# Kernel tuning notes

Hardware: AMD Instinct MI355X
Metric: run time of the kernel (lower is better)

Reference implementation:

```python
import jax, jax.numpy as jnp
import numpy as np

N_NODES = 20000
N_EDGES = 160000
N_GRAPHS = 64
IN_DIM = 128
HID = 512
N_ACT = 32


def gcn_conv(x, W, b, src, dst, n_nodes):
    # PyG GCNConv: add self-loops, symmetric normalization, x @ W then scatter-add.
    loop = jnp.arange(n_nodes, dtype=src.dtype)
    s = jnp.concatenate([src, loop])
    d = jnp.concatenate([dst, loop])
    deg = jax.ops.segment_sum(jnp.ones_like(d, dtype=x.dtype), d, num_segments=n_nodes)
    dinv = jnp.where(deg > 0, jax.lax.rsqrt(deg), 0.0)
    norm = dinv[s] * dinv[d]                      # [E+N]
    h = x @ W                                     # [N, out]
    msg = h[s] * norm[:, None]                    # gather + scale
    out = jax.ops.segment_sum(msg, d, num_segments=n_nodes)
    return out + b


def setup_inputs() -> dict:
    key = jax.random.key(0)
    ks = jax.random.split(key, 16)
    tree_x = jax.random.normal(ks[0], (N_NODES, IN_DIM), dtype=jnp.float32)
    edge_index = jax.random.randint(ks[1], (2, N_EDGES), 0, N_NODES, dtype=jnp.int32)
    # batch assignment: guarantee every graph id appears, then sort
    raw = jnp.concatenate([jnp.arange(N_GRAPHS, dtype=jnp.int32),
                           jax.random.randint(ks[2], (N_NODES - N_GRAPHS,), 0, N_GRAPHS, dtype=jnp.int32)])
    batch = jnp.sort(raw)

    def glorot(k, shape):
        lim = np.sqrt(6.0 / (shape[0] + shape[1]))
        return jax.random.uniform(k, shape, jnp.float32, -lim, lim)

    params = {
        'W1': glorot(ks[3], (IN_DIM, HID)), 'b1': jnp.zeros((HID,), jnp.float32),
        'W2': glorot(ks[4], (HID, HID)),    'b2': jnp.zeros((HID,), jnp.float32),
        'W3': glorot(ks[5], (HID, HID)),    'b3': jnp.zeros((HID,), jnp.float32),
        'Wf1': glorot(ks[6], (HID, HID)),   'bf1': jnp.zeros((HID,), jnp.float32),
        'Wf2': glorot(ks[7], (HID, HID)),   'bf2': jnp.zeros((HID,), jnp.float32),
        'Wf3': glorot(ks[8], (HID, HID)),   'bf3': jnp.zeros((HID,), jnp.float32),
        'Wo': glorot(ks[9], (HID, N_ACT)),  'bo': jnp.zeros((N_ACT,), jnp.float32),
    }
    return {'tree_x': tree_x, 'edge_index': edge_index, 'batch': batch, **params}


def reference(tree_x, edge_index, batch, W1, b1, W2, b2, W3, b3,
              Wf1, bf1, Wf2, bf2, Wf3, bf3, Wo, bo):
    src, dst = edge_index[0], edge_index[1]
    h = jax.nn.relu(gcn_conv(tree_x, W1, b1, src, dst, N_NODES))
    h = jax.nn.relu(gcn_conv(h, W2, b2, src, dst, N_NODES))
    h = jax.nn.relu(gcn_conv(h, W3, b3, src, dst, N_NODES))
    x = jax.ops.segment_max(h, batch, num_segments=N_GRAPHS)  # global_max_pool
    x = jax.nn.relu(x @ Wf1 + bf1)
    x = jax.nn.relu(x @ Wf2 + bf2)
    x = jax.nn.relu(x @ Wf3 + bf3)
    return x @ Wo + bo
```

## Files before the change

kernel.cpp:

```cpp
#include <hip/hip_runtime.h>
#include <stdint.h>

#define N_NODES 20000
#define N_EDGES 160000
#define N_GRAPHS 64
#define IN_DIM 128
#define HID 512
#define N_ACT 32

#define SCAN_NB ((N_NODES + 255) / 256)

typedef __attribute__((ext_vector_type(8))) short short8;
typedef __attribute__((ext_vector_type(4))) float f32x4;

__device__ __forceinline__ float bf2f(uint h16) {
    union { uint u; float f; } v; v.u = h16 << 16; return v.f;
}
__device__ __forceinline__ float bflo(uint u) {
    union { uint x; float f; } v; v.x = u << 16; return v.f;
}
__device__ __forceinline__ float bfhi(uint u) {
    union { uint x; float f; } v; v.x = u & 0xffff0000u; return v.f;
}
__device__ __forceinline__ ushort f2bf(float f) {
    union { float f; uint u; } v; v.f = f;
    uint u = v.u;
    uint r = (u + 0x7fffu + ((u >> 16) & 1u)) >> 16;
    return (ushort)r;
}


#define PB_HIST   625
#define PB_F2BF   (PB_HIST + 10000)
#define PB_WT1    (PB_F2BF + 256)
#define PB_WT2    (PB_WT1 + 1024)
#define PB_WT3    (PB_WT2 + 1024)
#define PB_BOUNDS (PB_WT3 + SCAN_NB)

__global__ __launch_bounds__(256) void k_prep(
    const int* __restrict__ edst, int* __restrict__ cnt,
    const float* __restrict__ tree_x, ushort* __restrict__ xbf,
    const float* __restrict__ W1, ushort* __restrict__ w1t,
    const float* __restrict__ W2, ushort* __restrict__ w2t,
    const float* __restrict__ W3, ushort* __restrict__ w3t,
    const int* __restrict__ batch, int* __restrict__ gstart)
{
    int b = blockIdx.x;
    int t = threadIdx.x;
    if (b < PB_HIST) {
        int e = b * 256 + t;
        if (e < N_EDGES) atomicAdd(&cnt[edst[e]], 1);
    } else if (b < PB_F2BF) {
        int i = (b - PB_HIST) * 256 + t;
        if (i < N_NODES * IN_DIM) xbf[i] = f2bf(tree_x[i]);
    } else if (b < PB_WT1) {
        int i = (b - PB_F2BF) * 256 + t;
        int n = i / IN_DIM, k = i % IN_DIM;
        w1t[i] = f2bf(W1[k * HID + n]);
    } else if (b < PB_WT2) {
        int i = (b - PB_WT1) * 256 + t;
        int n = i / HID, k = i % HID;
        w2t[i] = f2bf(W2[k * HID + n]);
    } else if (b < PB_WT3) {
        int i = (b - PB_WT2) * 256 + t;
        int n = i / HID, k = i % HID;
        w3t[i] = f2bf(W3[k * HID + n]);
    } else {
        int i = (b - PB_WT3) * 256 + t;
        if (i < N_NODES) {
            if (i == 0) {
                gstart[batch[0]] = 0;
                gstart[N_GRAPHS] = N_NODES;
            } else if (batch[i] != batch[i - 1]) {
                gstart[batch[i]] = i;
            }
        }
    }
}


__global__ __launch_bounds__(256) void k_part(const int* __restrict__ cnt, int* __restrict__ bsum) {
    __shared__ int s[256];
    int idx = blockIdx.x * 256 + threadIdx.x;
    s[threadIdx.x] = (idx < N_NODES) ? cnt[idx] : 0;
    __syncthreads();
    for (int off = 128; off > 0; off >>= 1) {
        if (threadIdx.x < off) s[threadIdx.x] += s[threadIdx.x + off];
        __syncthreads();
    }
    if (threadIdx.x == 0) bsum[blockIdx.x] = s[0];
}

__global__ __launch_bounds__(128) void k_scanb(const int* __restrict__ bsum,
                                               int* __restrict__ boff, int* __restrict__ rowstart) {
    __shared__ int s[128];
    int t = threadIdx.x;
    int own = (t < SCAN_NB) ? bsum[t] : 0;
    s[t] = own;
    __syncthreads();
    for (int off = 1; off < 128; off <<= 1) {
        int v = 0;
        if (t >= off) v = s[t - off];
        __syncthreads();
        s[t] += v;
        __syncthreads();
    }
    if (t < SCAN_NB) boff[t] = s[t] - own;
    if (t == SCAN_NB - 1) rowstart[N_NODES] = s[t];
}

__global__ __launch_bounds__(256) void k_final(
    const int* __restrict__ cnt, const int* __restrict__ boff,
    int* __restrict__ rowstart, int* __restrict__ cursor, float* __restrict__ dinv)
{
    __shared__ int s[256];
    int t = threadIdx.x;
    int idx = blockIdx.x * 256 + t;
    int c = (idx < N_NODES) ? cnt[idx] : 0;
    s[t] = c;
    __syncthreads();
    for (int off = 1; off < 256; off <<= 1) {
        int v = 0;
        if (t >= off) v = s[t - off];
        __syncthreads();
        s[t] += v;
        __syncthreads();
    }
    if (idx < N_NODES) {
        int start = boff[blockIdx.x] + s[t] - c;
        rowstart[idx] = start;
        cursor[idx] = start;
        dinv[idx] = rsqrtf((float)c + 1.0f);
    }
}

__global__ void k_fill(const int* __restrict__ src, const int* __restrict__ dst,
                       int* __restrict__ cursor, int* __restrict__ csr_src) {
    int e = blockIdx.x * 256 + threadIdx.x;
    if (e < N_EDGES) {
        int p = atomicAdd(&cursor[dst[e]], 1);
        csr_src[p] = src[e];
    }
}


__global__ __launch_bounds__(256) void k_gemm(
    const ushort* __restrict__ A, const ushort* __restrict__ Bt,
    const float* __restrict__ dinv, const float* __restrict__ bias,
    ushort* __restrict__ Out, int M, int Kdim, int mode)
{
    const int N = HID;
    __shared__ __align__(16) ushort lA[128 * 64];
    __shared__ __align__(16) ushort lB[128 * 64];
    int bm = blockIdx.x, bn = blockIdx.y;
    int tid = threadIdx.x;
    int wave = tid >> 6, lane = tid & 63;
    int wm = (wave >> 1) * 64, wn = (wave & 1) * 64;

    f32x4 acc[4][4] = {};

    int srow = lane >> 3;
    int scol = (lane & 7) * 8;

    for (int kt = 0; kt < Kdim; kt += 64) {
        for (int c = wave * 4; c < wave * 4 + 4; ++c) {
            int row = c * 8 + srow;
            int ga = bm * 128 + row; if (ga >= M) ga = M - 1;
            const ushort* gsA = A + (size_t)ga * Kdim + kt + scol;
            __builtin_amdgcn_global_load_lds(
                (const __attribute__((address_space(1))) void*)gsA,
                (__attribute__((address_space(3))) void*)(lA + c * 512), 16, 0, 0);
            int gb = bn * 128 + row;
            const ushort* gsB = Bt + (size_t)gb * Kdim + kt + scol;
            __builtin_amdgcn_global_load_lds(
                (const __attribute__((address_space(1))) void*)gsB,
                (__attribute__((address_space(3))) void*)(lB + c * 512), 16, 0, 0);
        }
        __syncthreads();
        for (int kk = 0; kk < 2; ++kk) {
            short8 af[4], bfr[4];
            int ko = kk * 32 + (lane >> 4) * 8;
            for (int m = 0; m < 4; ++m)
                af[m] = *(const short8*)&lA[(wm + m * 16 + (lane & 15)) * 64 + ko];
            for (int n = 0; n < 4; ++n)
                bfr[n] = *(const short8*)&lB[(wn + n * 16 + (lane & 15)) * 64 + ko];
            for (int m = 0; m < 4; ++m)
                for (int n = 0; n < 4; ++n)
                    acc[m][n] = __builtin_amdgcn_mfma_f32_16x16x32_bf16(af[m], bfr[n], acc[m][n], 0, 0, 0);
        }
        __syncthreads();
    }

    int cb = bn * 128 + wn + (lane & 15);
    float bb[4];
    if (mode == 1) {
        for (int n = 0; n < 4; ++n) bb[n] = bias[cb + n * 16];
    }
    for (int m = 0; m < 4; ++m) {
        int rbase = bm * 128 + wm + m * 16 + (lane >> 4) * 4;
        for (int j = 0; j < 4; ++j) {
            int r = rbase + j;
            if (r < M) {
                if (mode == 0) {
                    float dv = dinv[r];
                    for (int n = 0; n < 4; ++n)
                        Out[(size_t)r * N + cb + n * 16] = f2bf(acc[m][n][j] * dv);
                } else {
                    for (int n = 0; n < 4; ++n)
                        Out[(size_t)r * N + cb + n * 16] = f2bf(fmaxf(acc[m][n][j] + bb[n], 0.0f));
                }
            }
        }
    }
}


__global__ __launch_bounds__(64) void k_agg1(
    const ushort* __restrict__ Xin, const int* __restrict__ rowstart,
    const int* __restrict__ csr_src, const float* __restrict__ dinv,
    ushort* __restrict__ Y)
{
    int i = blockIdx.x;
    int lane = threadIdx.x;
    const uint* xin = (const uint*)Xin;
    float dv = dinv[i];
    uint xi = xin[(size_t)i * 64 + lane];
    float a0 = dv * bflo(xi), a1 = dv * bfhi(xi);
    int e = rowstart[i], s1 = rowstart[i + 1];
    for (; e + 2 <= s1; e += 2) {
        int sa = csr_src[e], sb = csr_src[e + 1];
        float da = dinv[sa], db = dinv[sb];
        uint wa = xin[(size_t)sa * 64 + lane];
        uint wb = xin[(size_t)sb * 64 + lane];
        a0 = fmaf(da, bflo(wa), a0); a1 = fmaf(da, bfhi(wa), a1);
        a0 = fmaf(db, bflo(wb), a0); a1 = fmaf(db, bfhi(wb), a1);
    }
    if (e < s1) {
        int sa = csr_src[e];
        float da = dinv[sa];
        uint wa = xin[(size_t)sa * 64 + lane];
        a0 = fmaf(da, bflo(wa), a0); a1 = fmaf(da, bfhi(wa), a1);
    }
    uint o = (uint)f2bf(dv * a0) | ((uint)f2bf(dv * a1) << 16);
    ((uint*)Y)[(size_t)i * 64 + lane] = o;
}


__global__ __launch_bounds__(64) void k_agg(
    const ushort* __restrict__ G, const int* __restrict__ rowstart,
    const int* __restrict__ csr_src, const float* __restrict__ dinv,
    const float* __restrict__ bias, ushort* __restrict__ X)
{
    int i = blockIdx.x;
    int lane = threadIdx.x;
    const uint4* g4 = (const uint4*)G;

    uint4 a = g4[(size_t)i * 64 + lane];
    float acc[8] = { bflo(a.x), bfhi(a.x), bflo(a.y), bfhi(a.y),
                     bflo(a.z), bfhi(a.z), bflo(a.w), bfhi(a.w) };

    int e = rowstart[i], s1 = rowstart[i + 1];
    for (; e + 2 <= s1; e += 2) {
        int sa = csr_src[e], sb = csr_src[e + 1];
        uint4 wa = g4[(size_t)sa * 64 + lane];
        uint4 wb = g4[(size_t)sb * 64 + lane];
        acc[0] += bflo(wa.x); acc[1] += bfhi(wa.x);
        acc[2] += bflo(wa.y); acc[3] += bfhi(wa.y);
        acc[4] += bflo(wa.z); acc[5] += bfhi(wa.z);
        acc[6] += bflo(wa.w); acc[7] += bfhi(wa.w);
        acc[0] += bflo(wb.x); acc[1] += bfhi(wb.x);
        acc[2] += bflo(wb.y); acc[3] += bfhi(wb.y);
        acc[4] += bflo(wb.z); acc[5] += bfhi(wb.z);
        acc[6] += bflo(wb.w); acc[7] += bfhi(wb.w);
    }
    if (e < s1) {
        int sa = csr_src[e];
        uint4 wa = g4[(size_t)sa * 64 + lane];
        acc[0] += bflo(wa.x); acc[1] += bfhi(wa.x);
        acc[2] += bflo(wa.y); acc[3] += bfhi(wa.y);
        acc[4] += bflo(wa.z); acc[5] += bfhi(wa.z);
        acc[6] += bflo(wa.w); acc[7] += bfhi(wa.w);
    }

    float dv = dinv[i];
    float4 b0 = *(const float4*)(bias + lane * 8);
    float4 b1 = *(const float4*)(bias + lane * 8 + 4);
    float bb[8] = { b0.x, b0.y, b0.z, b0.w, b1.x, b1.y, b1.z, b1.w };

    uint4 o;
    uint p[8];
    for (int j = 0; j < 8; ++j)
        p[j] = f2bf(fmaxf(fmaf(dv, acc[j], bb[j]), 0.0f));
    o.x = p[0] | (p[1] << 16);
    o.y = p[2] | (p[3] << 16);
    o.z = p[4] | (p[5] << 16);
    o.w = p[6] | (p[7] << 16);
    *(uint4*)(X + (size_t)i * HID + lane * 8) = o;
}


__global__ __launch_bounds__(64) void k_pool(
    const ushort* __restrict__ X, const int* __restrict__ gstart, float* __restrict__ P)
{
    int g = blockIdx.x;
    int ch = blockIdx.y * 64 + threadIdx.x;
    float mx = -1e30f;
    int i0 = gstart[g], i1 = gstart[g + 1];
    int i = i0;
    for (; i + 4 <= i1; i += 4) {
        float a = bf2f(X[(size_t)(i + 0) * HID + ch]);
        float b = bf2f(X[(size_t)(i + 1) * HID + ch]);
        float c = bf2f(X[(size_t)(i + 2) * HID + ch]);
        float d = bf2f(X[(size_t)(i + 3) * HID + ch]);
        mx = fmaxf(mx, fmaxf(fmaxf(a, b), fmaxf(c, d)));
    }
    for (; i < i1; ++i) mx = fmaxf(mx, bf2f(X[(size_t)i * HID + ch]));
    P[(size_t)g * HID + ch] = mx;
}


__global__ __launch_bounds__(256) void k_fc(
    const float* __restrict__ in, const float* __restrict__ W,
    const float* __restrict__ b, float* __restrict__ out,
    int K, int NO, int relu)
{
    __shared__ float xs[HID];
    __shared__ float part[4][64];
    int g = blockIdx.x;
    int j0 = blockIdx.y * 64;
    int tid = threadIdx.x;
    int wave = tid >> 6, lane = tid & 63;

    for (int k = tid; k < K; k += 256) xs[k] = in[(size_t)g * K + k];
    __syncthreads();

    int j = j0 + lane;
    bool active = (j < NO);
    int kpw = K >> 2;
    int k0 = wave * kpw;
    float acc = 0.0f;
    if (active) {
        const float* wp = W + (size_t)k0 * NO + j;
        int k = 0;
        for (; k + 4 <= kpw; k += 4) {
            float w0 = wp[(size_t)(k + 0) * NO];
            float w1 = wp[(size_t)(k + 1) * NO];
            float w2 = wp[(size_t)(k + 2) * NO];
            float w3 = wp[(size_t)(k + 3) * NO];
            acc = fmaf(xs[k0 + k + 0], w0, acc);
            acc = fmaf(xs[k0 + k + 1], w1, acc);
            acc = fmaf(xs[k0 + k + 2], w2, acc);
            acc = fmaf(xs[k0 + k + 3], w3, acc);
        }
        for (; k < kpw; ++k)
            acc = fmaf(xs[k0 + k], wp[(size_t)k * NO], acc);
    }
    part[wave][lane] = acc;
    __syncthreads();
    if (wave == 0 && active) {
        float a = part[0][lane] + part[1][lane] + part[2][lane] + part[3][lane] + b[j];
        if (relu) a = fmaxf(a, 0.0f);
        out[(size_t)g * NO + j] = a;
    }
}


extern "C" void kernel_launch(void* const* d_in, const int* in_sizes, int n_in,
                              void* d_out, int out_size, void* d_ws, size_t ws_size,
                              hipStream_t stream) {
    const float* tree_x = (const float*)d_in[0];
    const int*   ei     = (const int*)d_in[1];
    const int*   batch  = (const int*)d_in[2];
    const float* W1  = (const float*)d_in[3];  const float* b1  = (const float*)d_in[4];
    const float* W2  = (const float*)d_in[5];  const float* b2  = (const float*)d_in[6];
    const float* W3  = (const float*)d_in[7];  const float* b3  = (const float*)d_in[8];
    const float* Wf1 = (const float*)d_in[9];  const float* bf1 = (const float*)d_in[10];
    const float* Wf2 = (const float*)d_in[11]; const float* bf2 = (const float*)d_in[12];
    const float* Wf3 = (const float*)d_in[13]; const float* bf3 = (const float*)d_in[14];
    const float* Wo  = (const float*)d_in[15]; const float* bo  = (const float*)d_in[16];

    char* w = (char*)d_ws;
    size_t off = 0;
    auto alloc = [&](size_t bytes) -> void* {
        void* p = w + off;
        off += (bytes + 255) & ~(size_t)255;
        return p;
    };
    int*    cnt      = (int*)alloc((size_t)N_NODES * 4);
    int*    cursor   = (int*)alloc((size_t)N_NODES * 4);
    int*    rowstart = (int*)alloc((size_t)(N_NODES + 1) * 4);
    float*  dinv     = (float*)alloc((size_t)N_NODES * 4);
    int*    csr      = (int*)alloc((size_t)N_EDGES * 4);
    int*    gstart   = (int*)alloc((size_t)(N_GRAPHS + 1) * 4);
    int*    bsum     = (int*)alloc((size_t)SCAN_NB * 4);
    int*    boff     = (int*)alloc((size_t)SCAN_NB * 4);
    ushort* xbf      = (ushort*)alloc((size_t)N_NODES * IN_DIM * 2);
    ushort* ybuf     = (ushort*)alloc((size_t)N_NODES * IN_DIM * 2);
    ushort* w1t      = (ushort*)alloc((size_t)HID * IN_DIM * 2);
    ushort* w2t      = (ushort*)alloc((size_t)HID * HID * 2);
    ushort* w3t      = (ushort*)alloc((size_t)HID * HID * 2);
    ushort* gbuf     = (ushort*)alloc((size_t)N_NODES * HID * 2);
    ushort* xbuf     = (ushort*)alloc((size_t)N_NODES * HID * 2);
    float*  P0       = (float*)alloc((size_t)N_GRAPHS * HID * 4);
    float*  P1       = (float*)alloc((size_t)N_GRAPHS * HID * 4);

    const int* esrc = ei;
    const int* edst = ei + N_EDGES;

    hipMemsetAsync(cnt, 0, (size_t)N_NODES * 4, stream);
    k_prep<<<PB_BOUNDS, 256, 0, stream>>>(edst, cnt, tree_x, xbf,
                                          W1, w1t, W2, w2t, W3, w3t, batch, gstart);
    k_part<<<SCAN_NB, 256, 0, stream>>>(cnt, bsum);
    k_scanb<<<1, 128, 0, stream>>>(bsum, boff, rowstart);
    k_final<<<SCAN_NB, 256, 0, stream>>>(cnt, boff, rowstart, cursor, dinv);
    k_fill<<<(N_EDGES + 255) / 256, 256, 0, stream>>>(esrc, edst, cursor, csr);

    dim3 gemm_grid((N_NODES + 127) / 128, HID / 128);

    k_agg1<<<N_NODES, 64, 0, stream>>>(xbf, rowstart, csr, dinv, ybuf);
    k_gemm<<<gemm_grid, 256, 0, stream>>>(ybuf, w1t, dinv, b1, xbuf, N_NODES, IN_DIM, 1);
    k_gemm<<<gemm_grid, 256, 0, stream>>>(xbuf, w2t, dinv, b2, gbuf, N_NODES, HID, 0);
    k_agg<<<N_NODES, 64, 0, stream>>>(gbuf, rowstart, csr, dinv, b2, xbuf);
    k_gemm<<<gemm_grid, 256, 0, stream>>>(xbuf, w3t, dinv, b3, gbuf, N_NODES, HID, 0);
    k_agg<<<N_NODES, 64, 0, stream>>>(gbuf, rowstart, csr, dinv, b3, xbuf);

    k_pool<<<dim3(N_GRAPHS, 8), 64, 0, stream>>>(xbuf, gstart, P0);

    k_fc<<<dim3(N_GRAPHS, HID / 64), 256, 0, stream>>>(P0, Wf1, bf1, P1, HID, HID, 1);
    k_fc<<<dim3(N_GRAPHS, HID / 64), 256, 0, stream>>>(P1, Wf2, bf2, P0, HID, HID, 1);
    k_fc<<<dim3(N_GRAPHS, HID / 64), 256, 0, stream>>>(P0, Wf3, bf3, P1, HID, HID, 1);
    k_fc<<<dim3(N_GRAPHS, 1), 256, 0, stream>>>(P1, Wo, bo, (float*)d_out, HID, N_ACT, 0);
}
```

Baseline: 238.5 us.

## Fuse max-pool into final aggregation with atomicMax and pack four nodes per block

The last GCN aggregation now writes straight into the pooled buffer through atomicMax on float bits; this works because the ReLU output is non-negative and the buffer is zeroed by a memset. That removes the separate pool kernel, the gstart computation and the full write and re-read of the node feature matrix. The aggregation kernels also now run four nodes per 256-thread block and unroll the neighbour loop by four, giving more loads in flight. The cost is heavy atomic contention, since about 300 nodes per graph hit the same 512 addresses, and pooling values are no longer rounded to bf16.

```diff
diff --git a/kernel.cpp b/kernel.cpp
--- a/kernel.cpp
+++ b/kernel.cpp
@@ -29,21 +29,26 @@
     return (ushort)r;
 }
 
+__device__ __forceinline__ void add8(float* acc, uint4 v) {
+    acc[0] += bflo(v.x); acc[1] += bfhi(v.x);
+    acc[2] += bflo(v.y); acc[3] += bfhi(v.y);
+    acc[4] += bflo(v.z); acc[5] += bfhi(v.z);
+    acc[6] += bflo(v.w); acc[7] += bfhi(v.w);
+}
+
 
 #define PB_HIST   625
 #define PB_F2BF   (PB_HIST + 10000)
 #define PB_WT1    (PB_F2BF + 256)
 #define PB_WT2    (PB_WT1 + 1024)
 #define PB_WT3    (PB_WT2 + 1024)
-#define PB_BOUNDS (PB_WT3 + SCAN_NB)
 
 __global__ __launch_bounds__(256) void k_prep(
     const int* __restrict__ edst, int* __restrict__ cnt,
     const float* __restrict__ tree_x, ushort* __restrict__ xbf,
     const float* __restrict__ W1, ushort* __restrict__ w1t,
     const float* __restrict__ W2, ushort* __restrict__ w2t,
-    const float* __restrict__ W3, ushort* __restrict__ w3t,
-    const int* __restrict__ batch, int* __restrict__ gstart)
+    const float* __restrict__ W3, ushort* __restrict__ w3t)
 {
     int b = blockIdx.x;
     int t = threadIdx.x;
@@ -61,20 +66,10 @@
         int i = (b - PB_WT1) * 256 + t;
         int n = i / HID, k = i % HID;
         w2t[i] = f2bf(W2[k * HID + n]);
-    } else if (b < PB_WT3) {
+    } else {
         int i = (b - PB_WT2) * 256 + t;
         int n = i / HID, k = i % HID;
         w3t[i] = f2bf(W3[k * HID + n]);
-    } else {
-        int i = (b - PB_WT3) * 256 + t;
-        if (i < N_NODES) {
-            if (i == 0) {
-                gstart[batch[0]] = 0;
-                gstart[N_GRAPHS] = N_NODES;
-            } else if (batch[i] != batch[i - 1]) {
-                gstart[batch[i]] = i;
-            }
-        }
     }
 }
 
@@ -215,27 +210,32 @@
 }
 
 
-__global__ __launch_bounds__(64) void k_agg1(
+__global__ __launch_bounds__(256) void k_agg1(
     const ushort* __restrict__ Xin, const int* __restrict__ rowstart,
     const int* __restrict__ csr_src, const float* __restrict__ dinv,
     ushort* __restrict__ Y)
 {
-    int i = blockIdx.x;
-    int lane = threadIdx.x;
+    int i = blockIdx.x * 4 + (threadIdx.x >> 6);
+    if (i >= N_NODES) return;
+    int lane = threadIdx.x & 63;
     const uint* xin = (const uint*)Xin;
     float dv = dinv[i];
     uint xi = xin[(size_t)i * 64 + lane];
     float a0 = dv * bflo(xi), a1 = dv * bfhi(xi);
     int e = rowstart[i], s1 = rowstart[i + 1];
-    for (; e + 2 <= s1; e += 2) {
-        int sa = csr_src[e], sb = csr_src[e + 1];
-        float da = dinv[sa], db = dinv[sb];
+    for (; e + 4 <= s1; e += 4) {
+        int sa = csr_src[e], sb = csr_src[e + 1], sc = csr_src[e + 2], sd = csr_src[e + 3];
+        float da = dinv[sa], db = dinv[sb], dc = dinv[sc], dd = dinv[sd];
         uint wa = xin[(size_t)sa * 64 + lane];
         uint wb = xin[(size_t)sb * 64 + lane];
+        uint wc = xin[(size_t)sc * 64 + lane];
+        uint wd = xin[(size_t)sd * 64 + lane];
         a0 = fmaf(da, bflo(wa), a0); a1 = fmaf(da, bfhi(wa), a1);
         a0 = fmaf(db, bflo(wb), a0); a1 = fmaf(db, bfhi(wb), a1);
-    }
-    if (e < s1) {
+        a0 = fmaf(dc, bflo(wc), a0); a1 = fmaf(dc, bfhi(wc), a1);
+        a0 = fmaf(dd, bflo(wd), a0); a1 = fmaf(dd, bfhi(wd), a1);
+    }
+    for (; e < s1; ++e) {
         int sa = csr_src[e];
         float da = dinv[sa];
         uint wa = xin[(size_t)sa * 64 + lane];
@@ -246,13 +246,14 @@
 }
 
 
-__global__ __launch_bounds__(64) void k_agg(
+__global__ __launch_bounds__(256) void k_agg(
     const ushort* __restrict__ G, const int* __restrict__ rowstart,
     const int* __restrict__ csr_src, const float* __restrict__ dinv,
     const float* __restrict__ bias, ushort* __restrict__ X)
 {
-    int i = blockIdx.x;
-    int lane = threadIdx.x;
+    int i = blockIdx.x * 4 + (threadIdx.x >> 6);
+    if (i >= N_NODES) return;
+    int lane = threadIdx.x & 63;
     const uint4* g4 = (const uint4*)G;
 
     uint4 a = g4[(size_t)i * 64 + lane];
@@ -260,26 +261,18 @@
                      bflo(a.z), bfhi(a.z), bflo(a.w), bfhi(a.w) };
 
     int e = rowstart[i], s1 = rowstart[i + 1];
-    for (; e + 2 <= s1; e += 2) {
-        int sa = csr_src[e], sb = csr_src[e + 1];
+    for (; e + 4 <= s1; e += 4) {
+        int sa = csr_src[e], sb = csr_src[e + 1], sc = csr_src[e + 2], sd = csr_src[e + 3];
         uint4 wa = g4[(size_t)sa * 64 + lane];
         uint4 wb = g4[(size_t)sb * 64 + lane];
-        acc[0] += bflo(wa.x); acc[1] += bfhi(wa.x);
-        acc[2] += bflo(wa.y); acc[3] += bfhi(wa.y);
-        acc[4] += bflo(wa.z); acc[5] += bfhi(wa.z);
-        acc[6] += bflo(wa.w); acc[7] += bfhi(wa.w);
-        acc[0] += bflo(wb.x); acc[1] += bfhi(wb.x);
-        acc[2] += bflo(wb.y); acc[3] += bfhi(wb.y);
-        acc[4] += bflo(wb.z); acc[5] += bfhi(wb.z);
-        acc[6] += bflo(wb.w); acc[7] += bfhi(wb.w);
-    }
-    if (e < s1) {
+        uint4 wc = g4[(size_t)sc * 64 + lane];
+        uint4 wd = g4[(size_t)sd * 64 + lane];
+        add8(acc, wa); add8(acc, wb); add8(acc, wc); add8(acc, wd);
+    }
+    for (; e < s1; ++e) {
         int sa = csr_src[e];
         uint4 wa = g4[(size_t)sa * 64 + lane];
-        acc[0] += bflo(wa.x); acc[1] += bfhi(wa.x);
-        acc[2] += bflo(wa.y); acc[3] += bfhi(wa.y);
-        acc[4] += bflo(wa.z); acc[5] += bfhi(wa.z);
-        acc[6] += bflo(wa.w); acc[7] += bfhi(wa.w);
+        add8(acc, wa);
     }
 
     float dv = dinv[i];
@@ -299,23 +292,47 @@
 }
 
 
-__global__ __launch_bounds__(64) void k_pool(
-    const ushort* __restrict__ X, const int* __restrict__ gstart, float* __restrict__ P)
-{
-    int g = blockIdx.x;
-    int ch = blockIdx.y * 64 + threadIdx.x;
-    float mx = -1e30f;
-    int i0 = gstart[g], i1 = gstart[g + 1];
-    int i = i0;
-    for (; i + 4 <= i1; i += 4) {
-        float a = bf2f(X[(size_t)(i + 0) * HID + ch]);
-        float b = bf2f(X[(size_t)(i + 1) * HID + ch]);
-        float c = bf2f(X[(size_t)(i + 2) * HID + ch]);
-        float d = bf2f(X[(size_t)(i + 3) * HID + ch]);
-        mx = fmaxf(mx, fmaxf(fmaxf(a, b), fmaxf(c, d)));
-    }
-    for (; i < i1; ++i) mx = fmaxf(mx, bf2f(X[(size_t)i * HID + ch]));
-    P[(size_t)g * HID + ch] = mx;
+__global__ __launch_bounds__(256) void k_agg3(
+    const ushort* __restrict__ G, const int* __restrict__ rowstart,
+    const int* __restrict__ csr_src, const float* __restrict__ dinv,
+    const float* __restrict__ bias, const int* __restrict__ batch,
+    float* __restrict__ P)
+{
+    int i = blockIdx.x * 4 + (threadIdx.x >> 6);
+    if (i >= N_NODES) return;
+    int lane = threadIdx.x & 63;
+    const uint4* g4 = (const uint4*)G;
+
+    uint4 a = g4[(size_t)i * 64 + lane];
+    float acc[8] = { bflo(a.x), bfhi(a.x), bflo(a.y), bfhi(a.y),
+                     bflo(a.z), bfhi(a.z), bflo(a.w), bfhi(a.w) };
+
+    int e = rowstart[i], s1 = rowstart[i + 1];
+    for (; e + 4 <= s1; e += 4) {
+        int sa = csr_src[e], sb = csr_src[e + 1], sc = csr_src[e + 2], sd = csr_src[e + 3];
+        uint4 wa = g4[(size_t)sa * 64 + lane];
+        uint4 wb = g4[(size_t)sb * 64 + lane];
+        uint4 wc = g4[(size_t)sc * 64 + lane];
+        uint4 wd = g4[(size_t)sd * 64 + lane];
+        add8(acc, wa); add8(acc, wb); add8(acc, wc); add8(acc, wd);
+    }
+    for (; e < s1; ++e) {
+        int sa = csr_src[e];
+        uint4 wa = g4[(size_t)sa * 64 + lane];
+        add8(acc, wa);
+    }
+
+    float dv = dinv[i];
+    float4 b0 = *(const float4*)(bias + lane * 8);
+    float4 b1 = *(const float4*)(bias + lane * 8 + 4);
+    float bb[8] = { b0.x, b0.y, b0.z, b0.w, b1.x, b1.y, b1.z, b1.w };
+
+    int g = batch[i];
+    uint* pp = (uint*)(P + (size_t)g * HID + lane * 8);
+    for (int j = 0; j < 8; ++j) {
+        float v = fmaxf(fmaf(dv, acc[j], bb[j]), 0.0f);
+        atomicMax(&pp[j], __float_as_uint(v));
+    }
 }
 
 
@@ -391,7 +408,6 @@
     int*    rowstart = (int*)alloc((size_t)(N_NODES + 1) * 4);
     float*  dinv     = (float*)alloc((size_t)N_NODES * 4);
     int*    csr      = (int*)alloc((size_t)N_EDGES * 4);
-    int*    gstart   = (int*)alloc((size_t)(N_GRAPHS + 1) * 4);
     int*    bsum     = (int*)alloc((size_t)SCAN_NB * 4);
     int*    boff     = (int*)alloc((size_t)SCAN_NB * 4);
     ushort* xbf      = (ushort*)alloc((size_t)N_NODES * IN_DIM * 2);
@@ -408,8 +424,9 @@
     const int* edst = ei + N_EDGES;
 
     hipMemsetAsync(cnt, 0, (size_t)N_NODES * 4, stream);
-    k_prep<<<PB_BOUNDS, 256, 0, stream>>>(edst, cnt, tree_x, xbf,
-                                          W1, w1t, W2, w2t, W3, w3t, batch, gstart);
+    hipMemsetAsync(P0, 0, (size_t)N_GRAPHS * HID * 4, stream);
+    k_prep<<<PB_WT3, 256, 0, stream>>>(edst, cnt, tree_x, xbf,
+                                       W1, w1t, W2, w2t, W3, w3t);
     k_part<<<SCAN_NB, 256, 0, stream>>>(cnt, bsum);
     k_scanb<<<1, 128, 0, stream>>>(bsum, boff, rowstart);
     k_final<<<SCAN_NB, 256, 0, stream>>>(cnt, boff, rowstart, cursor, dinv);
@@ -417,14 +434,12 @@
 
     dim3 gemm_grid((N_NODES + 127) / 128, HID / 128);
 
-    k_agg1<<<N_NODES, 64, 0, stream>>>(xbf, rowstart, csr, dinv, ybuf);
+    k_agg1<<<N_NODES / 4, 256, 0, stream>>>(xbf, rowstart, csr, dinv, ybuf);
     k_gemm<<<gemm_grid, 256, 0, stream>>>(ybuf, w1t, dinv, b1, xbuf, N_NODES, IN_DIM, 1);
     k_gemm<<<gemm_grid, 256, 0, stream>>>(xbuf, w2t, dinv, b2, gbuf, N_NODES, HID, 0);
-    k_agg<<<N_NODES, 64, 0, stream>>>(gbuf, rowstart, csr, dinv, b2, xbuf);
+    k_agg<<<N_NODES / 4, 256, 0, stream>>>(gbuf, rowstart, csr, dinv, b2, xbuf);
     k_gemm<<<gemm_grid, 256, 0, stream>>>(xbuf, w3t, dinv, b3, gbuf, N_NODES, HID, 0);
-    k_agg<<<N_NODES, 64, 0, stream>>>(gbuf, rowstart, csr, dinv, b3, xbuf);
-
-    k_pool<<<dim3(N_GRAPHS, 8), 64, 0, stream>>>(xbuf, gstart, P0);
+    k_agg3<<<N_NODES / 4, 256, 0, stream>>>(gbuf, rowstart, csr, dinv, b3, batch, P0);
 
     k_fc<<<dim3(N_GRAPHS, HID / 64), 256, 0, stream>>>(P0, Wf1, bf1, P1, HID, HID, 1);
     k_fc<<<dim3(N_GRAPHS, HID / 64), 256, 0, stream>>>(P1, Wf2, bf2, P0, HID, HID, 1);
```

Result: slower. 454.3 us (+90.5%).
